# Kernel optimization log

Measured on AMD Instinct MI355X. Metric: run time of the kernel, lower is better.

Reference implementation:

```python
import jax, jax.numpy as jnp
import numpy as np
import math

D, H, DH = 1024, 16, 64
QR, KR, VR = 256, 256, 256
B, T = 2, 2048


def setup_inputs() -> dict:
    key = jax.random.key(0)
    ks = jax.random.split(key, 10)
    s = 0.02
    return {
        "x": jax.random.normal(ks[0], (B, T, D), dtype=jnp.float32),
        "attention_mask": jnp.ones((B, T), dtype=jnp.int32),
        # torch nn.Linear weights are [out_features, in_features]
        "Wq_down": jax.random.normal(ks[1], (QR, D), dtype=jnp.float32) * s,
        "Wk_down": jax.random.normal(ks[2], (KR, D), dtype=jnp.float32) * s,
        "Wv_down": jax.random.normal(ks[3], (VR, D), dtype=jnp.float32) * s,
        "Wq_up": jax.random.normal(ks[4], (D, QR), dtype=jnp.float32) * s,
        "Wk_up": jax.random.normal(ks[5], (D, KR), dtype=jnp.float32) * s,
        "Wv_up": jax.random.normal(ks[6], (D, VR), dtype=jnp.float32) * s,
        "Wo": jax.random.normal(ks[7], (D, D), dtype=jnp.float32) * s,
        "bo": jnp.zeros((D,), dtype=jnp.float32),
    }


def reference(x, attention_mask, Wq_down, Wk_down, Wv_down, Wq_up, Wk_up, Wv_up, Wo, bo):
    Bx, Tx, d = x.shape
    # latent down-projections (no bias)
    Q_lat = x @ Wq_down.T            # [B,T,QR]
    K_lat = x @ Wk_down.T            # [B,S,KR]  (S == T, no past_kv)
    V_lat = x @ Wv_down.T            # [B,S,VR]
    S = K_lat.shape[1]

    # per-head views of up-projection weights: view(H, d_h, r).transpose(1,2) -> (H, r, d_h)
    Uq_h = Wq_up.reshape(H, DH, QR).transpose(0, 2, 1)   # [H,QR,DH]
    Uk_h = Wk_up.reshape(H, DH, KR).transpose(0, 2, 1)   # [H,KR,DH]
    Uv_h = Wv_up.reshape(H, DH, VR).transpose(0, 2, 1)   # [H,VR,DH]

    # absorbed Q/K matrix
    Mabs = jnp.einsum('hqd,hkd->hqk', Uq_h, Uk_h) * (1.0 / math.sqrt(DH))  # [H,QR,KR]

    # low-rank attention logits directly from latents
    logits = jnp.einsum('btq,hqk,bsk->bhts', Q_lat, Mabs, K_lat)  # [B,H,T,S]

    # causal mask (P = S - T = 0)
    P = S - Tx
    i = jnp.arange(Tx)[:, None]
    j = jnp.arange(S)[None, :]
    future = (j > P + i)[None, None, :, :]                 # [1,1,T,S]
    key_pad = (attention_mask == 0)[:, None, None, :]      # [B,1,1,S]
    neg_inf = jnp.float32(-jnp.inf)
    logits = jnp.where(future | key_pad, neg_inf, logits)

    attn = jax.nn.softmax(logits.astype(jnp.float32), axis=-1)
    attn = jnp.nan_to_num(attn).astype(x.dtype)

    V_up = jnp.einsum('bsr,hrd->bhsd', V_lat, Uv_h)        # [B,H,S,DH]
    ctx = jnp.einsum('bhts,bhsd->bhtd', attn, V_up)        # [B,H,T,DH]
    ctx = ctx.transpose(0, 2, 1, 3).reshape(Bx, Tx, H * DH)
    out = ctx @ Wo.T + bo
    return out
```

## Files before the change

### kernel.cpp

```cpp
#include <hip/hip_runtime.h>

using f32x4 = __attribute__((ext_vector_type(4))) float;
using s16x8 = __attribute__((ext_vector_type(8))) short;
using u16x4 = __attribute__((ext_vector_type(4))) unsigned short;
using u32 = unsigned int;

static __device__ __forceinline__ unsigned short f2bf(float f) {
  u32 u = __builtin_bit_cast(u32, f);
  u = (u + 0x7fffu + ((u >> 16) & 1u)) >> 16;
  return (unsigned short)u;
}

static __device__ __forceinline__ void gload_lds16(const void* g, void* l) {
  __builtin_amdgcn_global_load_lds((const __attribute__((address_space(1))) void*)g,
                                   (__attribute__((address_space(3))) void*)l, 16, 0, 0);
}

__global__ void k_cvt(const float* __restrict__ src, unsigned short* __restrict__ dst, int n4) {
  int i = blockIdx.x * blockDim.x + threadIdx.x;
  if (i >= n4) return;
  float4 v = reinterpret_cast<const float4*>(src)[i];
  u16x4 o;
  o[0] = f2bf(v.x); o[1] = f2bf(v.y); o[2] = f2bf(v.z); o[3] = f2bf(v.w);
  reinterpret_cast<u16x4*>(dst)[i] = o;
}

__global__ void k_mabs(const float* __restrict__ Wqu, const float* __restrict__ Wku,
                       unsigned short* __restrict__ MabsT) {
  __shared__ float sq[64][65];
  __shared__ float sk[64][65];
  int h = blockIdx.z, q0 = blockIdx.x * 64, k0 = blockIdx.y * 64;
  int t = threadIdx.x;
  for (int r = 0; r < 16; ++r) {
    int d = r * 4 + (t >> 6);
    int c = t & 63;
    sq[d][c] = Wqu[(size_t)(h * 64 + d) * 256 + q0 + c];
    sk[d][c] = Wku[(size_t)(h * 64 + d) * 256 + k0 + c];
  }
  __syncthreads();
  int kk = t >> 2, qs = t & 3;
  float acc[16];
#pragma unroll
  for (int j = 0; j < 16; ++j) acc[j] = 0.f;
  for (int d = 0; d < 64; ++d) {
    float kv = sk[d][kk];
#pragma unroll
    for (int j = 0; j < 16; ++j) acc[j] += kv * sq[d][qs + 4 * j];
  }
#pragma unroll
  for (int j = 0; j < 16; ++j)
    MabsT[((size_t)(h * 256 + k0 + kk)) * 256 + q0 + qs + 4 * j] = f2bf(acc[j] * 0.125f);
}

__global__ __launch_bounds__(256) void k_gemm(
    const unsigned short* __restrict__ A, int lda,
    const unsigned short* __restrict__ B0, int ldb, long bstride,
    void* __restrict__ C, const float* __restrict__ bias,
    int M, int N, int K, int ldc, int mode) {
  __shared__ unsigned short As[128 * 32];
  __shared__ unsigned short Bs[128 * 32];
  int bz = blockIdx.z;
  const unsigned short* B = B0 + (size_t)bz * bstride;
  int row0 = blockIdx.x * 128, col0 = blockIdx.y * 128;
  int t = threadIdx.x;
  int lane = t & 63, w = t >> 6;
  int wr = w >> 1, wc = w & 1;
  int lc = lane & 15, kr = (lane >> 4) * 8;

  f32x4 acc[4][4];
#pragma unroll
  for (int m = 0; m < 4; ++m)
#pragma unroll
    for (int n = 0; n < 4; ++n) acc[m][n] = (f32x4){0.f, 0.f, 0.f, 0.f};

  for (int k0 = 0; k0 < K; k0 += 32) {
    __syncthreads();
#pragma unroll
    for (int c = 0; c < 2; ++c) {
      int f = (c * 256 + t) * 16;
      int r = f >> 6, kb = (f & 63) >> 1;
      gload_lds16(A + (size_t)(row0 + r) * lda + k0 + kb, (char*)As + c * 4096 + w * 1024);
    }
#pragma unroll
    for (int c = 0; c < 2; ++c) {
      int f = (c * 256 + t) * 16;
      int r = f >> 6, kb = (f & 63) >> 1;
      gload_lds16(B + (size_t)(col0 + r) * ldb + k0 + kb, (char*)Bs + c * 4096 + w * 1024);
    }
    asm volatile("s_waitcnt vmcnt(0)" ::: "memory");
    __syncthreads();

    s16x8 af[4], bf[4];
#pragma unroll
    for (int m = 0; m < 4; ++m)
      af[m] = *(const s16x8*)&As[(wr * 64 + m * 16 + lc) * 32 + kr];
#pragma unroll
    for (int n = 0; n < 4; ++n)
      bf[n] = *(const s16x8*)&Bs[(wc * 64 + n * 16 + lc) * 32 + kr];
#pragma unroll
    for (int m = 0; m < 4; ++m)
#pragma unroll
      for (int n = 0; n < 4; ++n)
        acc[m][n] = __builtin_amdgcn_mfma_f32_16x16x32_bf16(af[m], bf[n], acc[m][n], 0, 0, 0);
  }

  int rbase = row0 + wr * 64, cbase = col0 + wc * 64;
  int lr4 = (lane >> 4) * 4;
#pragma unroll
  for (int m = 0; m < 4; ++m)
#pragma unroll
    for (int n = 0; n < 4; ++n)
#pragma unroll
      for (int r = 0; r < 4; ++r) {
        int grow = rbase + m * 16 + lr4 + r;
        int gcol = cbase + n * 16 + lc;
        float v = acc[m][n][r];
        if (mode == 0) {
          ((unsigned short*)C)[(size_t)grow * ldc + gcol] = f2bf(v);
        } else if (mode == 1) {
          ((float*)C)[(size_t)grow * ldc + gcol] = v + bias[gcol];
        } else if (mode == 2) {
          int b_ = grow >> 11, s_ = grow & 2047;
          ((unsigned short*)C)[((size_t)b_ * N + gcol) * 2048 + s_] = f2bf(v);
        } else {
          int b_ = grow >> 11, t_ = grow & 2047;
          ((unsigned short*)C)[(((size_t)(b_ * 16 + bz)) * 2048 + t_) * 256 + gcol] = f2bf(v);
        }
      }
}

__global__ __launch_bounds__(256, 2) void k_attn(
    const unsigned short* __restrict__ Qabs, const unsigned short* __restrict__ Lat,
    const unsigned short* __restrict__ VupT, unsigned short* __restrict__ ctx) {
  __shared__ unsigned short Ks[2][32 * 264];
  __shared__ unsigned short Vs[2][64 * 40];
  __shared__ unsigned short Pl[4][16 * 40];

  const int bx = blockIdx.x;
  const int bh = blockIdx.y;
  const int b = bh >> 4, h = bh & 15;
  const int t = threadIdx.x, lane = t & 63, w = t >> 6;
  const int lrow = lane & 15, hi = lane >> 4;
  const int kr = hi * 8;

  const unsigned short* Q = Qabs + (size_t)bh * 2048 * 256;
  const unsigned short* Kp = Lat + (size_t)b * 2048 * 768 + 256;
  const unsigned short* Vp = VupT + ((size_t)b * 1024 + h * 64) * 2048;
  unsigned short* Op = ctx + (size_t)b * 2048 * 1024 + h * 64;

  uint4 kstg[4];
  uint4 vstg;
  const int krr0 = t >> 5;
  const int kcc = t & 31;
  const int vrr = t >> 2, vcc = t & 3;

#define K_ISSUE(s0g)                                                           \
  {                                                                            \
    _Pragma("unroll") for (int c = 0; c < 4; ++c) kstg[c] =                    \
        *(const uint4*)(Kp + (size_t)((s0g) + c * 8 + krr0) * 768 + kcc * 8);  \
    vstg = *(const uint4*)(Vp + (size_t)vrr * 2048 + (s0g) + vcc * 8);         \
  }
#define KV_WRITE(bufi)                                                         \
  {                                                                            \
    _Pragma("unroll") for (int c = 0; c < 4; ++c)                              \
        *(uint4*)&Ks[bufi][(c * 8 + krr0) * 264 + kcc * 8] = kstg[c];          \
    *(uint4*)&Vs[bufi][vrr * 40 + vcc * 8] = vstg;                             \
  }

  for (int seg = 0; seg < 2; ++seg) {
    const int tb = (seg == 0 ? bx : 31 - bx) * 64;
    const int qb = tb + w * 16;

    s16x8 qf[8];
#pragma unroll
    for (int kk = 0; kk < 8; ++kk)
      qf[kk] = *(const s16x8*)&Q[(size_t)(qb + lrow) * 256 + kk * 32 + kr];

    f32x4 o[4];
#pragma unroll
    for (int dt = 0; dt < 4; ++dt) o[dt] = (f32x4){0.f, 0.f, 0.f, 0.f};
    float mrow[4], lsum[4];
    int myrow[4];
#pragma unroll
    for (int r = 0; r < 4; ++r) {
      mrow[r] = -1e30f;
      lsum[r] = 0.f;
      myrow[r] = qb + hi * 4 + r;
    }

    K_ISSUE(0)
    KV_WRITE(0)
    __syncthreads();

    const int nsteps = tb / 32 + 2;
    for (int st = 0; st < nsteps; ++st) {
      const int buf = st & 1;
      const int s0 = st * 32;
      const bool pfn = (st + 1 < nsteps);
      if (pfn) { K_ISSUE(s0 + 32) }

      s16x8 kfa[2][8];
#pragma unroll
      for (int hf = 0; hf < 2; ++hf)
#pragma unroll
        for (int kk = 0; kk < 8; ++kk)
          kfa[hf][kk] = *(const s16x8*)&Ks[buf][(hf * 16 + lrow) * 264 + kk * 32 + kr];

      f32x4 sf[2];
      sf[0] = (f32x4){0.f, 0.f, 0.f, 0.f};
      sf[1] = (f32x4){0.f, 0.f, 0.f, 0.f};
#pragma unroll
      for (int kk = 0; kk < 8; ++kk) {
        sf[0] = __builtin_amdgcn_mfma_f32_16x16x32_bf16(qf[kk], kfa[0][kk], sf[0], 0, 0, 0);
        sf[1] = __builtin_amdgcn_mfma_f32_16x16x32_bf16(qf[kk], kfa[1][kk], sf[1], 0, 0, 0);
      }

#pragma unroll
      for (int r = 0; r < 4; ++r) {
        int q = myrow[r];
        if (s0 + lrow > q) sf[0][r] = -1e30f;
        if (s0 + 16 + lrow > q) sf[1][r] = -1e30f;
        float mloc = fmaxf(sf[0][r], sf[1][r]);
        if (!__all(mloc <= mrow[r] + 8.f)) {
          float mx = mloc;
#pragma unroll
          for (int off = 1; off < 16; off <<= 1) mx = fmaxf(mx, __shfl_xor(mx, off));
          float mnew = fmaxf(mrow[r], mx);
          float scale = __expf(mrow[r] - mnew);
          mrow[r] = mnew;
          lsum[r] *= scale;
#pragma unroll
          for (int dt = 0; dt < 4; ++dt) o[dt][r] *= scale;
        }
        float p0 = __expf(sf[0][r] - mrow[r]);
        float p1 = __expf(sf[1][r] - mrow[r]);
        sf[0][r] = p0;
        sf[1][r] = p1;
        lsum[r] += p0 + p1;
      }
#pragma unroll
      for (int r = 0; r < 4; ++r) {
        Pl[w][(hi * 4 + r) * 40 + lrow] = f2bf(sf[0][r]);
        Pl[w][(hi * 4 + r) * 40 + 16 + lrow] = f2bf(sf[1][r]);
      }
      asm volatile("s_waitcnt lgkmcnt(0)" ::: "memory");
      __builtin_amdgcn_sched_barrier(0);

      s16x8 pf = *(const s16x8*)&Pl[w][lrow * 40 + kr];
      s16x8 vfa[4];
#pragma unroll
      for (int dt = 0; dt < 4; ++dt)
        vfa[dt] = *(const s16x8*)&Vs[buf][(dt * 16 + lrow) * 40 + kr];
#pragma unroll
      for (int dt = 0; dt < 4; ++dt)
        o[dt] = __builtin_amdgcn_mfma_f32_16x16x32_bf16(pf, vfa[dt], o[dt], 0, 0, 0);

      if (pfn) { KV_WRITE(buf ^ 1) }
      __syncthreads();
    }

#pragma unroll
    for (int r = 0; r < 4; ++r) {
      float ls = lsum[r];
#pragma unroll
      for (int off = 1; off < 16; off <<= 1) ls += __shfl_xor(ls, off);
      lsum[r] = ls;
    }
#pragma unroll
    for (int dt = 0; dt < 4; ++dt)
#pragma unroll
      for (int r = 0; r < 4; ++r) {
        float v = o[dt][r] / lsum[r];
        Op[(size_t)myrow[r] * 1024 + dt * 16 + lrow] = f2bf(v);
      }
    __syncthreads();
  }
#undef K_ISSUE
#undef KV_WRITE
}

extern "C" void kernel_launch(void* const* d_in, const int* in_sizes, int n_in,
                              void* d_out, int out_size, void* d_ws, size_t ws_size,
                              hipStream_t stream) {
  const float* x = (const float*)d_in[0];
  const float* Wqd = (const float*)d_in[2];
  const float* Wkd = (const float*)d_in[3];
  const float* Wvd = (const float*)d_in[4];
  const float* Wqu = (const float*)d_in[5];
  const float* Wku = (const float*)d_in[6];
  const float* Wvu = (const float*)d_in[7];
  const float* Wo = (const float*)d_in[8];
  const float* bo = (const float*)d_in[9];
  float* out = (float*)d_out;

  char* ws = (char*)d_ws;
  unsigned short* xb = (unsigned short*)(ws);
  unsigned short* Wdb = (unsigned short*)(ws + 8388608);
  unsigned short* Wvub = (unsigned short*)(ws + 9961472);
  unsigned short* Wob = (unsigned short*)(ws + 10485760);
  unsigned short* MabsT = (unsigned short*)(ws + 12582912);
  unsigned short* Lat = (unsigned short*)(ws + 14680064);
  unsigned short* Qabs = (unsigned short*)(ws + 20971520);
  unsigned short* VupT = (unsigned short*)(ws + 54525952);
  unsigned short* ctx = (unsigned short*)(ws + 62914560);

  k_cvt<<<4096, 256, 0, stream>>>(x, xb, 1048576);
  k_cvt<<<256, 256, 0, stream>>>(Wqd, Wdb, 65536);
  k_cvt<<<256, 256, 0, stream>>>(Wkd, Wdb + 262144, 65536);
  k_cvt<<<256, 256, 0, stream>>>(Wvd, Wdb + 524288, 65536);
  k_cvt<<<256, 256, 0, stream>>>(Wvu, Wvub, 65536);
  k_cvt<<<1024, 256, 0, stream>>>(Wo, Wob, 262144);
  k_mabs<<<dim3(4, 4, 16), 256, 0, stream>>>(Wqu, Wku, MabsT);
  k_gemm<<<dim3(32, 6, 1), 256, 0, stream>>>(xb, 1024, Wdb, 1024, 0, Lat, nullptr,
                                             4096, 768, 1024, 768, 0);
  k_gemm<<<dim3(32, 2, 16), 256, 0, stream>>>(Lat, 768, MabsT, 256, 65536, Qabs, nullptr,
                                              4096, 256, 256, 0, 3);
  k_gemm<<<dim3(32, 8, 1), 256, 0, stream>>>(Lat + 512, 768, Wvub, 256, 0, VupT, nullptr,
                                             4096, 1024, 256, 0, 2);
  k_attn<<<dim3(16, 32), 256, 0, stream>>>(Qabs, Lat, VupT, ctx);
  k_gemm<<<dim3(32, 8, 1), 256, 0, stream>>>(ctx, 1024, Wob, 1024, 0, out, bo,
                                             4096, 1024, 1024, 1024, 1);
}
```

Measured before the change: 293.8 us.

## Fuse conversion kernels, compute VupT via transposed GEMM, rebalance causal attention tiles

Merges the six fp32-to-bf16 conversion launches into one kernel that picks its source by index range. The V up-projection is now computed as a swapped-operand GEMM that writes VupT row-major, so the scattered transposed-store mode is no longer needed. The attention grid changes from 16 blocks, each pairing two query tiles, to 22 blocks with a new pairing that gives the heaviest causal tiles a block of their own. This targets launch overhead, uncoalesced stores and tail imbalance, at the cost of a different VupT layout the attention kernel must index.

```diff
diff --git a/kernel.cpp b/kernel.cpp
--- a/kernel.cpp
+++ b/kernel.cpp
@@ -16,13 +16,25 @@
                                    (__attribute__((address_space(3))) void*)l, 16, 0, 0);
 }
 
-__global__ void k_cvt(const float* __restrict__ src, unsigned short* __restrict__ dst, int n4) {
+__global__ void k_cvt_all(const float* __restrict__ x, const float* __restrict__ Wqd,
+                          const float* __restrict__ Wkd, const float* __restrict__ Wvd,
+                          const float* __restrict__ Wvu, const float* __restrict__ Wo,
+                          unsigned short* __restrict__ xb, unsigned short* __restrict__ Wdb,
+                          unsigned short* __restrict__ Wvub, unsigned short* __restrict__ Wob) {
   int i = blockIdx.x * blockDim.x + threadIdx.x;
-  if (i >= n4) return;
-  float4 v = reinterpret_cast<const float4*>(src)[i];
+  const float* s;
+  unsigned short* d;
+  int off;
+  if (i < 1048576) { s = x; d = xb; off = i; }
+  else if (i < 1114112) { s = Wqd; d = Wdb; off = i - 1048576; }
+  else if (i < 1179648) { s = Wkd; d = Wdb + 262144; off = i - 1114112; }
+  else if (i < 1245184) { s = Wvd; d = Wdb + 524288; off = i - 1179648; }
+  else if (i < 1310720) { s = Wvu; d = Wvub; off = i - 1245184; }
+  else { s = Wo; d = Wob; off = i - 1310720; }
+  float4 v = reinterpret_cast<const float4*>(s)[off];
   u16x4 o;
   o[0] = f2bf(v.x); o[1] = f2bf(v.y); o[2] = f2bf(v.z); o[3] = f2bf(v.w);
-  reinterpret_cast<u16x4*>(dst)[i] = o;
+  reinterpret_cast<u16x4*>(d)[off] = o;
 }
 
 __global__ void k_mabs(const float* __restrict__ Wqu, const float* __restrict__ Wku,
@@ -119,9 +131,6 @@
           ((unsigned short*)C)[(size_t)grow * ldc + gcol] = f2bf(v);
         } else if (mode == 1) {
           ((float*)C)[(size_t)grow * ldc + gcol] = v + bias[gcol];
-        } else if (mode == 2) {
-          int b_ = grow >> 11, s_ = grow & 2047;
-          ((unsigned short*)C)[((size_t)b_ * N + gcol) * 2048 + s_] = f2bf(v);
         } else {
           int b_ = grow >> 11, t_ = grow & 2047;
           ((unsigned short*)C)[(((size_t)(b_ * 16 + bz)) * 2048 + t_) * 256 + gcol] = f2bf(v);
@@ -145,8 +154,13 @@
 
   const unsigned short* Q = Qabs + (size_t)bh * 2048 * 256;
   const unsigned short* Kp = Lat + (size_t)b * 2048 * 768 + 256;
-  const unsigned short* Vp = VupT + ((size_t)b * 1024 + h * 64) * 2048;
+  const unsigned short* Vp = VupT + (size_t)(h * 64) * 4096 + b * 2048;
   unsigned short* Op = ctx + (size_t)b * 2048 * 1024 + h * 64;
+
+  int tile0, tile1, ntiles;
+  if (bx <= 10) { tile0 = 31 - bx; tile1 = 0; ntiles = 1; }
+  else if (bx == 11) { tile0 = 10; tile1 = 0; ntiles = 1; }
+  else { tile0 = bx - 12; tile1 = 32 - bx; ntiles = 2; }
 
   uint4 kstg[4];
   uint4 vstg;
@@ -158,7 +172,7 @@
   {                                                                            \
     _Pragma("unroll") for (int c = 0; c < 4; ++c) kstg[c] =                    \
         *(const uint4*)(Kp + (size_t)((s0g) + c * 8 + krr0) * 768 + kcc * 8);  \
-    vstg = *(const uint4*)(Vp + (size_t)vrr * 2048 + (s0g) + vcc * 8);         \
+    vstg = *(const uint4*)(Vp + (size_t)vrr * 4096 + (s0g) + vcc * 8);         \
   }
 #define KV_WRITE(bufi)                                                         \
   {                                                                            \
@@ -167,8 +181,8 @@
     *(uint4*)&Vs[bufi][vrr * 40 + vcc * 8] = vstg;                             \
   }
 
-  for (int seg = 0; seg < 2; ++seg) {
-    const int tb = (seg == 0 ? bx : 31 - bx) * 64;
+  for (int seg = 0; seg < ntiles; ++seg) {
+    const int tb = (seg == 0 ? tile0 : tile1) * 64;
     const int qb = tb + w * 16;
 
     s16x8 qf[8];
@@ -304,20 +318,15 @@
   unsigned short* VupT = (unsigned short*)(ws + 54525952);
   unsigned short* ctx = (unsigned short*)(ws + 62914560);
 
-  k_cvt<<<4096, 256, 0, stream>>>(x, xb, 1048576);
-  k_cvt<<<256, 256, 0, stream>>>(Wqd, Wdb, 65536);
-  k_cvt<<<256, 256, 0, stream>>>(Wkd, Wdb + 262144, 65536);
-  k_cvt<<<256, 256, 0, stream>>>(Wvd, Wdb + 524288, 65536);
-  k_cvt<<<256, 256, 0, stream>>>(Wvu, Wvub, 65536);
-  k_cvt<<<1024, 256, 0, stream>>>(Wo, Wob, 262144);
+  k_cvt_all<<<6144, 256, 0, stream>>>(x, Wqd, Wkd, Wvd, Wvu, Wo, xb, Wdb, Wvub, Wob);
   k_mabs<<<dim3(4, 4, 16), 256, 0, stream>>>(Wqu, Wku, MabsT);
   k_gemm<<<dim3(32, 6, 1), 256, 0, stream>>>(xb, 1024, Wdb, 1024, 0, Lat, nullptr,
                                              4096, 768, 1024, 768, 0);
   k_gemm<<<dim3(32, 2, 16), 256, 0, stream>>>(Lat, 768, MabsT, 256, 65536, Qabs, nullptr,
-                                              4096, 256, 256, 0, 3);
-  k_gemm<<<dim3(32, 8, 1), 256, 0, stream>>>(Lat + 512, 768, Wvub, 256, 0, VupT, nullptr,
-                                             4096, 1024, 256, 0, 2);
-  k_attn<<<dim3(16, 32), 256, 0, stream>>>(Qabs, Lat, VupT, ctx);
+                                              4096, 256, 256, 0, 2);
+  k_gemm<<<dim3(8, 32, 1), 256, 0, stream>>>(Wvub, 256, Lat + 512, 768, 0, VupT, nullptr,
+                                             1024, 4096, 256, 4096, 0);
+  k_attn<<<dim3(22, 32), 256, 0, stream>>>(Qabs, Lat, VupT, ctx);
   k_gemm<<<dim3(32, 8, 1), 256, 0, stream>>>(ctx, 1024, Wob, 1024, 0, out, bo,
                                              4096, 1024, 1024, 1024, 1);
 }
```

After: 359.2 us. 1.22x slower.
